# Performance work log

Measured on AMD Instinct MI355X. Metric: run time of the kernel, lower is better.

The kernel has to match this reference:

```python
import jax, jax.numpy as jnp
import numpy as np

NUM_HEADS = 16
ROPE_THETA = 10000.0


def _rope_angles(seq_len, head_dim, dtype):
    # lucidrains rotary_embedding_torch: freqs = theta^(-2i/d) for i in 0..d/2,
    # angles = pos * freq, then each angle repeated twice along last dim (interleaved pairs).
    inv_freq = 1.0 / (ROPE_THETA ** (jnp.arange(0, head_dim, 2, dtype=jnp.float32) / head_dim))
    angles = jnp.arange(seq_len, dtype=jnp.float32)[:, None] * inv_freq  # [N, D/2]
    return jnp.repeat(angles, 2, axis=-1).astype(dtype)  # [N, D]


def _rotate_half(t):
    # interleaved pairs: (x0, x1) -> (-x1, x0)
    t1 = t[..., ::2]
    t2 = t[..., 1::2]
    return jnp.stack([-t2, t1], axis=-1).reshape(t.shape)


def _apply_rope(t, cos, sin):
    # t: [B, H, N, D]; cos/sin: [N, D]
    return t * cos + _rotate_half(t) * sin


def setup_inputs() -> dict:
    key = jax.random.key(0)
    ks = jax.random.split(key, 5)
    B, N, C = 4, 1024, 1024
    return {
        "x": jax.random.normal(ks[0], (B, N, C), dtype=jnp.float32),
        "w_qkv": jax.random.normal(ks[1], (C, 3 * C), dtype=jnp.float32) * (C ** -0.5),
        "b_qkv": jax.random.normal(ks[2], (3 * C,), dtype=jnp.float32) * 0.02,
        "w_proj": jax.random.normal(ks[3], (C, C), dtype=jnp.float32) * (C ** -0.5),
        "b_proj": jax.random.normal(ks[4], (C,), dtype=jnp.float32) * 0.02,
    }


def reference(x, w_qkv, b_qkv, w_proj, b_proj):
    B, N, C = x.shape
    H = NUM_HEADS
    D = C // H

    qkv = x @ w_qkv + b_qkv  # [B, N, 3C]
    qkv = qkv.reshape(B, N, 3, H, D).transpose(2, 0, 3, 1, 4)  # [3, B, H, N, D]
    q, k, v = qkv[0], qkv[1], qkv[2]

    ang = _rope_angles(N, D, x.dtype)
    cos, sin = jnp.cos(ang), jnp.sin(ang)
    q = _apply_rope(q, cos, sin)
    k = _apply_rope(k, cos, sin)

    scale = D ** -0.5  # SDPA default scale
    scores = jnp.einsum("bhqd,bhkd->bhqk", q, k) * scale
    attn = jax.nn.softmax(scores, axis=-1)
    out = jnp.einsum("bhqk,bhkd->bhqd", attn, v)  # [B, H, N, D]

    out = out.transpose(0, 2, 1, 3).reshape(B, N, C)
    return out @ w_proj + b_proj
```

## Files before the change

### kernel.cpp

```cpp
#include <hip/hip_runtime.h>
#include <math.h>

#define BB 4
#define NN 1024
#define CC 1024
#define HH 16
#define DD 64
#define N3 3072

typedef __attribute__((ext_vector_type(8))) short bf16x8;
typedef __attribute__((ext_vector_type(8))) _Float16 f16x8;
typedef __attribute__((ext_vector_type(4))) _Float16 f16x4;
typedef __attribute__((ext_vector_type(4))) float f32x4;

struct ushort4_t { unsigned short x, y, z, w; };

static __device__ __forceinline__ unsigned short f2b(float f) {
    union { float f; unsigned int u; } v; v.f = f;
    unsigned int r = (v.u + 0x7fffu + ((v.u >> 16) & 1u)) >> 16;
    return (unsigned short)r;
}

static __device__ __forceinline__ void ldg_lds16(const void* g, void* l) {
    __builtin_amdgcn_global_load_lds(
        (const __attribute__((address_space(1))) unsigned int*)g,
        (__attribute__((address_space(3))) unsigned int*)l, 16, 0, 0);
}

__global__ __launch_bounds__(256) void prep(const float* __restrict__ x,
                                            const float* __restrict__ wq,
                                            const float* __restrict__ wp,
                                            _Float16* __restrict__ Xh,
                                            _Float16* __restrict__ Wqt,
                                            _Float16* __restrict__ Wpt,
                                            float* __restrict__ ct,
                                            float* __restrict__ st) {
    const int blk = blockIdx.x;
    const int t = threadIdx.x;
    if (blk < 4096) {
        int tid = blk * 256 + t;
        float4 v = ((const float4*)x)[tid];
        f16x4 o = {(_Float16)v.x, (_Float16)v.y, (_Float16)v.z, (_Float16)v.w};
        ((f16x4*)Xh)[tid] = o;
    } else if (blk < 5632) {
        int idx = blk - 4096;
        int n  = (idx % 12) * 256 + t;
        int k0 = (idx / 12) * 8;
        f16x8 o;
        #pragma unroll
        for (int kk = 0; kk < 8; kk++)
            o[kk] = (_Float16)wq[(size_t)(k0 + kk) * N3 + n];
        *(f16x8*)(Wqt + (size_t)n * 1024 + k0) = o;
    } else if (blk < 6144) {
        int idx = blk - 5632;
        int n  = (idx % 4) * 256 + t;
        int k0 = (idx / 4) * 8;
        f16x8 o;
        #pragma unroll
        for (int kk = 0; kk < 8; kk++)
            o[kk] = (_Float16)wp[(size_t)(k0 + kk) * 1024 + n];
        *(f16x8*)(Wpt + (size_t)n * 1024 + k0) = o;
    } else {
        int tid = (blk - 6144) * 256 + t;
        int n = tid >> 5, i = tid & 31;
        double ang = (double)n * exp2(-(double)i * (13.287712379549449 / 32.0));
        ct[tid] = (float)cos(ang);
        st[tid] = (float)sin(ang);
    }
}

static __device__ __forceinline__ void gemm_body_128(const char* gA, const char* gB,
                                                     int m0, int n0,
                                                     _Float16* As, _Float16* Bs,
                                                     int w, int lane, int ln, int qd,
                                                     int wm, int wn, f32x4 acc[4][4]) {
    const int r8 = lane >> 3;
    const int xorc = ((lane & 7) ^ r8) * 16;
    for (int k0 = 0; k0 < 1024; k0 += 64) {
        #pragma unroll
        for (int c = 0; c < 4; c++) {
            int rr = w * 32 + c * 8 + r8;
            ldg_lds16(gA + (size_t)(m0 + rr) * 2048 + k0 * 2 + xorc,
                      &As[(w * 32 + c * 8) * 64]);
            ldg_lds16(gB + (size_t)(n0 + rr) * 2048 + k0 * 2 + xorc,
                      &Bs[(w * 32 + c * 8) * 64]);
        }
        __syncthreads();
        #pragma unroll
        for (int kc = 0; kc < 2; kc++) {
            f16x8 af[4], bf[4];
            #pragma unroll
            for (int i = 0; i < 4; i++)
                af[i] = *(const f16x8*)&As[(wm + i * 16 + ln) * 64 +
                                           (((kc * 4 + qd) ^ (ln & 7)) * 8)];
            #pragma unroll
            for (int j = 0; j < 4; j++)
                bf[j] = *(const f16x8*)&Bs[(wn + j * 16 + ln) * 64 +
                                           (((kc * 4 + qd) ^ (ln & 7)) * 8)];
            #pragma unroll
            for (int i = 0; i < 4; i++)
                #pragma unroll
                for (int j = 0; j < 4; j++)
                    acc[i][j] = __builtin_amdgcn_mfma_f32_16x16x32_f16(af[i], bf[j],
                                                                       acc[i][j], 0, 0, 0);
        }
        __syncthreads();
    }
}

__global__ __launch_bounds__(256) void qkv_mfma(const _Float16* __restrict__ Ah,
                                                const _Float16* __restrict__ Bt,
                                                const float* __restrict__ bias,
                                                const float* __restrict__ cost,
                                                const float* __restrict__ sint,
                                                unsigned short* __restrict__ Q,
                                                unsigned short* __restrict__ K,
                                                unsigned short* __restrict__ Vtg) {
    __shared__ __align__(16) _Float16 As[128 * 64];
    __shared__ __align__(16) _Float16 Bs[128 * 64];
    const int t = threadIdx.x;
    const int lane = t & 63;
    const int w = t >> 6;
    const int ln = lane & 15, qd = lane >> 4;
    const int n0 = blockIdx.x * 128;
    const int m0 = blockIdx.y * 128;
    const int wm = (w >> 1) * 64, wn = (w & 1) * 64;

    f32x4 acc[4][4];
    #pragma unroll
    for (int i = 0; i < 4; i++)
        #pragma unroll
        for (int j = 0; j < 4; j++) acc[i][j] = (f32x4){0.f, 0.f, 0.f, 0.f};

    gemm_body_128((const char*)Ah, (const char*)Bt, m0, n0, As, Bs,
                  w, lane, ln, qd, wm, wn, acc);

    const int s = n0 >> 10;
    const int h = ((n0 + wn) >> 6) & 15;
    if (s < 2) {
        unsigned short* dst = (s == 0) ? Q : K;
        const float sc0 = (s == 0) ? 0.125f : 1.0f;
        #pragma unroll
        for (int i = 0; i < 4; i++) {
            #pragma unroll
            for (int reg = 0; reg < 4; reg++) {
                int row = m0 + wm + i * 16 + qd * 4 + reg;
                int b = row >> 10, n = row & 1023;
                size_t obase = (((size_t)(b * HH + h)) * NN + n) * DD;
                #pragma unroll
                for (int j = 0; j < 4; j++) {
                    int d = j * 16 + ln;
                    float v = acc[i][j][reg] + bias[n0 + wn + d];
                    float pv = __shfl_xor(v, 1);
                    float cs = cost[n * 32 + (d >> 1)];
                    float sn = sint[n * 32 + (d >> 1)];
                    float outv = ((d & 1) ? (v * cs + pv * sn) : (v * cs - pv * sn)) * sc0;
                    dst[obase + d] = f2b(outv);
                }
            }
        }
    } else {
        #pragma unroll
        for (int i = 0; i < 4; i++) {
            int row0 = m0 + wm + i * 16 + qd * 4;
            int b = row0 >> 10, n = row0 & 1023;
            size_t tbase = ((size_t)(b * HH + h)) * DD * NN + n;
            #pragma unroll
            for (int j = 0; j < 4; j++) {
                int d = j * 16 + ln;
                float bb = bias[n0 + wn + d];
                ushort4_t pk;
                pk.x = f2b(acc[i][j][0] + bb);
                pk.y = f2b(acc[i][j][1] + bb);
                pk.z = f2b(acc[i][j][2] + bb);
                pk.w = f2b(acc[i][j][3] + bb);
                *(ushort4_t*)&Vtg[tbase + (size_t)d * NN] = pk;
            }
        }
    }
}

__global__ __launch_bounds__(256) void attn_flash(const unsigned short* __restrict__ Qb,
                                                  const unsigned short* __restrict__ Kb,
                                                  const unsigned short* __restrict__ Vtg,
                                                  _Float16* __restrict__ AO) {
    __shared__ __align__(16) unsigned short Ks[3][64 * 64];
    __shared__ __align__(16) unsigned short Vt[2][64 * 64];
    __shared__ __align__(16) unsigned short Ps[4][16 * 64];

    const int t    = threadIdx.x;
    const int lane = t & 63;
    const int w    = t >> 6;
    const int ln   = lane & 15;
    const int qd   = lane >> 4;
    const int bq   = blockIdx.x;
    const int h    = blockIdx.y;
    const int b    = blockIdx.z;
    const size_t base = (size_t)(b * HH + h) * NN * DD;
    const char* Kc = (const char*)(Kb + base);
    const char* Vc = (const char*)(Vtg + base);
    const int xorc = ((lane & 7) ^ (lane >> 3)) * 16;
    const int r8   = lane >> 3;
    const int wrow = w * 16;

    bf16x8 qf0, qf1;
    {
        const unsigned short* qp = Qb + base + (size_t)(bq * 64 + wrow + ln) * DD + qd * 8;
        qf0 = *(const bf16x8*)qp;
        qf1 = *(const bf16x8*)(qp + 32);
    }

    f32x4 o[5];
    #pragma unroll
    for (int x = 0; x < 5; x++) o[x] = (f32x4){0.f, 0.f, 0.f, 0.f};

    bf16x8 onesf;
    #pragma unroll
    for (int x = 0; x < 8; x++) onesf[x] = (short)0x3F80;

    #pragma unroll
    for (int tile = 0; tile < 3; tile++)
        #pragma unroll
        for (int c = 0; c < 2; c++) {
            int rr = wrow + c * 8 + r8;
            ldg_lds16(Kc + (size_t)(tile * 64 + rr) * 128 + xorc,
                      &Ks[tile][(wrow + c * 8) * 64]);
        }
    #pragma unroll
    for (int tile = 0; tile < 2; tile++)
        #pragma unroll
        for (int c = 0; c < 2; c++) {
            int rr = wrow + c * 8 + r8;
            ldg_lds16(Vc + (size_t)rr * 2048 + (size_t)tile * 128 + xorc,
                      &Vt[tile][(wrow + c * 8) * 64]);
        }
    __syncthreads();

    f32x4 scur[4];
    {
        const unsigned short* KsB = Ks[0];
        #pragma unroll
        for (int j = 0; j < 4; j++) {
            f32x4 sj = {0.f, 0.f, 0.f, 0.f};
            bf16x8 k0f = *(const bf16x8*)&KsB[(ln + 16 * j) * 64 + ((qd ^ (ln & 7)) * 8)];
            bf16x8 k1f = *(const bf16x8*)&KsB[(ln + 16 * j) * 64 + (((4 + qd) ^ (ln & 7)) * 8)];
            sj = __builtin_amdgcn_mfma_f32_16x16x32_bf16(qf0, k0f, sj, 0, 0, 0);
            sj = __builtin_amdgcn_mfma_f32_16x16x32_bf16(qf1, k1f, sj, 0, 0, 0);
            scur[j] = sj;
        }
    }

    const float C1 = 1.44269504f;
    const float C0 = -16.0f * 1.44269504f;

    #pragma unroll
    for (int tt = 0; tt < 16; tt++) {
        f32x4 snext[4];
        if (tt < 15) {
            const unsigned short* KsB = Ks[(tt + 1) % 3];
            #pragma unroll
            for (int j = 0; j < 4; j++) {
                f32x4 sj = {0.f, 0.f, 0.f, 0.f};
                bf16x8 k0f = *(const bf16x8*)&KsB[(ln + 16 * j) * 64 + ((qd ^ (ln & 7)) * 8)];
                bf16x8 k1f = *(const bf16x8*)&KsB[(ln + 16 * j) * 64 + (((4 + qd) ^ (ln & 7)) * 8)];
                sj = __builtin_amdgcn_mfma_f32_16x16x32_bf16(qf0, k0f, sj, 0, 0, 0);
                sj = __builtin_amdgcn_mfma_f32_16x16x32_bf16(qf1, k1f, sj, 0, 0, 0);
                snext[j] = sj;
            }
        }

        unsigned short* PsB = &Ps[w][0];
        #pragma unroll
        for (int j = 0; j < 4; j++) {
            #pragma unroll
            for (int r = 0; r < 4; r++) {
                float p = exp2f(fmaf(scur[j][r], C1, C0));
                union { float f; unsigned int u; } cv; cv.f = p;
                int m = qd * 4 + r;
                PsB[m * 64 + ((((ln >> 3) + 2 * j) ^ (m & 7)) * 8) + (ln & 7)] =
                    (unsigned short)((cv.u + 0x8000u) >> 16);
            }
        }

        {
            const unsigned short* VtB = Vt[tt & 1];
            bf16x8 pf0 = *(const bf16x8*)&PsB[ln * 64 + ((qd ^ (ln & 7)) * 8)];
            bf16x8 pf1 = *(const bf16x8*)&PsB[ln * 64 + (((4 + qd) ^ (ln & 7)) * 8)];
            #pragma unroll
            for (int j = 0; j < 4; j++) {
                bf16x8 v0f = *(const bf16x8*)&VtB[(ln + 16 * j) * 64 + ((qd ^ (ln & 7)) * 8)];
                bf16x8 v1f = *(const bf16x8*)&VtB[(ln + 16 * j) * 64 + (((4 + qd) ^ (ln & 7)) * 8)];
                o[j] = __builtin_amdgcn_mfma_f32_16x16x32_bf16(pf0, v0f, o[j], 0, 0, 0);
                o[j] = __builtin_amdgcn_mfma_f32_16x16x32_bf16(pf1, v1f, o[j], 0, 0, 0);
            }
            o[4] = __builtin_amdgcn_mfma_f32_16x16x32_bf16(pf0, onesf, o[4], 0, 0, 0);
            o[4] = __builtin_amdgcn_mfma_f32_16x16x32_bf16(pf1, onesf, o[4], 0, 0, 0);
        }

        __syncthreads();

        if (tt <= 12) {
            int tile = tt + 3;
            #pragma unroll
            for (int c = 0; c < 2; c++) {
                int rr = wrow + c * 8 + r8;
                ldg_lds16(Kc + (size_t)(tile * 64 + rr) * 128 + xorc,
                          &Ks[tt % 3][(wrow + c * 8) * 64]);
            }
        }
        if (tt <= 13) {
            int tile = tt + 2;
            #pragma unroll
            for (int c = 0; c < 2; c++) {
                int rr = wrow + c * 8 + r8;
                ldg_lds16(Vc + (size_t)rr * 2048 + (size_t)tile * 128 + xorc,
                          &Vt[tt & 1][(wrow + c * 8) * 64]);
            }
        }

        #pragma unroll
        for (int j = 0; j < 4; j++) scur[j] = snext[j];
    }

    #pragma unroll
    for (int r = 0; r < 4; r++) {
        float inv = 1.0f / o[4][r];
        int q = bq * 64 + wrow + qd * 4 + r;
        _Float16* op = AO + (((size_t)b * NN + q) * HH + h) * DD + ln;
        op[0]  = (_Float16)(o[0][r] * inv);
        op[16] = (_Float16)(o[1][r] * inv);
        op[32] = (_Float16)(o[2][r] * inv);
        op[48] = (_Float16)(o[3][r] * inv);
    }
}

__global__ __launch_bounds__(256) void proj_mfma(const _Float16* __restrict__ Ah,
                                                 const _Float16* __restrict__ Bt,
                                                 const float* __restrict__ bias,
                                                 float* __restrict__ out) {
    __shared__ __align__(16) _Float16 As[128 * 64];
    __shared__ __align__(16) _Float16 Bs[128 * 64];
    const int t = threadIdx.x;
    const int lane = t & 63;
    const int w = t >> 6;
    const int ln = lane & 15, qd = lane >> 4;
    const int n0 = blockIdx.x * 128;
    const int m0 = blockIdx.y * 128;
    const int wm = (w >> 1) * 64, wn = (w & 1) * 64;

    f32x4 acc[4][4];
    #pragma unroll
    for (int i = 0; i < 4; i++)
        #pragma unroll
        for (int j = 0; j < 4; j++) acc[i][j] = (f32x4){0.f, 0.f, 0.f, 0.f};

    gemm_body_128((const char*)Ah, (const char*)Bt, m0, n0, As, Bs,
                  w, lane, ln, qd, wm, wn, acc);

    #pragma unroll
    for (int i = 0; i < 4; i++) {
        #pragma unroll
        for (int reg = 0; reg < 4; reg++) {
            int row = m0 + wm + i * 16 + qd * 4 + reg;
            #pragma unroll
            for (int j = 0; j < 4; j++) {
                int col = n0 + wn + j * 16 + ln;
                out[(size_t)row * 1024 + col] = acc[i][j][reg] + bias[col];
            }
        }
    }
}

extern "C" void kernel_launch(void* const* d_in, const int* in_sizes, int n_in,
                              void* d_out, int out_size, void* d_ws, size_t ws_size,
                              hipStream_t stream) {
    const float* x      = (const float*)d_in[0];
    const float* w_qkv  = (const float*)d_in[1];
    const float* b_qkv  = (const float*)d_in[2];
    const float* w_proj = (const float*)d_in[3];
    const float* b_proj = (const float*)d_in[4];
    float* out = (float*)d_out;

    char* ws = (char*)d_ws;
    _Float16* Xh   = (_Float16*)(ws);
    _Float16* Wqt  = (_Float16*)(ws + (8u << 20));
    _Float16* Wpt  = (_Float16*)(ws + (14u << 20));
    unsigned short* Q  = (unsigned short*)(ws + (16u << 20));
    unsigned short* K  = (unsigned short*)(ws + (24u << 20));
    unsigned short* Vt = (unsigned short*)(ws + (32u << 20));
    _Float16* AOh  = (_Float16*)(ws + (40u << 20));
    float* cost    = (float*)(ws + (48u << 20));
    float* sint    = (float*)(ws + (48u << 20) + (128u << 10));

    prep<<<6272, 256, 0, stream>>>(x, w_qkv, w_proj, Xh, Wqt, Wpt, cost, sint);
    qkv_mfma<<<dim3(24, 32), 256, 0, stream>>>(Xh, Wqt, b_qkv, cost, sint, Q, K, Vt);
    attn_flash<<<dim3(16, 16, 4), 256, 0, stream>>>(Q, K, Vt, AOh);
    proj_mfma<<<dim3(8, 32), 256, 0, stream>>>(AOh, Wpt, b_proj, out);
}
```

Before: 199.2 us.

## Double-buffer GEMM LDS tiles with register-staged global prefetch

Replaces the direct global-to-LDS loads in the shared GEMM body with register-staged loads. Two LDS buffers are used so the next K tile is written while the current one is consumed, and the tile after that is prefetched into registers. This cuts the sync count to one barrier per K step and overlaps global latency with MFMA work in both the QKV and projection GEMMs. In exchange, LDS use doubles to 64KB per block and register pressure rises, which may lower occupancy.

```diff
diff --git a/kernel.cpp b/kernel.cpp
--- a/kernel.cpp
+++ b/kernel.cpp
@@ -12,6 +12,7 @@
 typedef __attribute__((ext_vector_type(8))) _Float16 f16x8;
 typedef __attribute__((ext_vector_type(4))) _Float16 f16x4;
 typedef __attribute__((ext_vector_type(4))) float f32x4;
+typedef __attribute__((ext_vector_type(4))) unsigned int u32x4;
 
 struct ushort4_t { unsigned short x, y, z, w; };
 
@@ -69,33 +70,54 @@
     }
 }
 
-static __device__ __forceinline__ void gemm_body_128(const char* gA, const char* gB,
-                                                     int m0, int n0,
-                                                     _Float16* As, _Float16* Bs,
-                                                     int w, int lane, int ln, int qd,
-                                                     int wm, int wn, f32x4 acc[4][4]) {
-    const int r8 = lane >> 3;
-    const int xorc = ((lane & 7) ^ r8) * 16;
-    for (int k0 = 0; k0 < 1024; k0 += 64) {
-        #pragma unroll
-        for (int c = 0; c < 4; c++) {
-            int rr = w * 32 + c * 8 + r8;
-            ldg_lds16(gA + (size_t)(m0 + rr) * 2048 + k0 * 2 + xorc,
-                      &As[(w * 32 + c * 8) * 64]);
-            ldg_lds16(gB + (size_t)(n0 + rr) * 2048 + k0 * 2 + xorc,
-                      &Bs[(w * 32 + c * 8) * 64]);
-        }
-        __syncthreads();
+static __device__ __forceinline__ void gemm_body_pipe(const char* gA, const char* gB,
+                                                      int m0, int n0,
+                                                      _Float16* As0, _Float16* As1,
+                                                      _Float16* Bs0, _Float16* Bs1,
+                                                      int tid, int ln, int qd,
+                                                      int wm, int wn, f32x4 acc[4][4]) {
+    const int lrow   = tid >> 3;
+    const int lchunk = tid & 7;
+    const int swz    = (lchunk ^ (lrow & 7)) * 8;
+
+    u32x4 pa[4], pb[4];
+
+    #pragma unroll
+    for (int c = 0; c < 4; c++) {
+        size_t ra = (size_t)(m0 + c * 32 + lrow) * 2048 + lchunk * 16;
+        size_t rb = (size_t)(n0 + c * 32 + lrow) * 2048 + lchunk * 16;
+        pa[c] = *(const u32x4*)(gA + ra);
+        pb[c] = *(const u32x4*)(gB + rb);
+    }
+    #pragma unroll
+    for (int c = 0; c < 4; c++) {
+        *(u32x4*)&As0[(c * 32 + lrow) * 64 + swz] = pa[c];
+        *(u32x4*)&Bs0[(c * 32 + lrow) * 64 + swz] = pb[c];
+    }
+    #pragma unroll
+    for (int c = 0; c < 4; c++) {
+        size_t ra = (size_t)(m0 + c * 32 + lrow) * 2048 + 128 + lchunk * 16;
+        size_t rb = (size_t)(n0 + c * 32 + lrow) * 2048 + 128 + lchunk * 16;
+        pa[c] = *(const u32x4*)(gA + ra);
+        pb[c] = *(const u32x4*)(gB + rb);
+    }
+    __syncthreads();
+
+    #pragma unroll
+    for (int t = 0; t < 16; t++) {
+        const _Float16* Ac = (t & 1) ? As1 : As0;
+        const _Float16* Bc = (t & 1) ? Bs1 : Bs0;
+
         #pragma unroll
         for (int kc = 0; kc < 2; kc++) {
             f16x8 af[4], bf[4];
             #pragma unroll
             for (int i = 0; i < 4; i++)
-                af[i] = *(const f16x8*)&As[(wm + i * 16 + ln) * 64 +
+                af[i] = *(const f16x8*)&Ac[(wm + i * 16 + ln) * 64 +
                                            (((kc * 4 + qd) ^ (ln & 7)) * 8)];
             #pragma unroll
             for (int j = 0; j < 4; j++)
-                bf[j] = *(const f16x8*)&Bs[(wn + j * 16 + ln) * 64 +
+                bf[j] = *(const f16x8*)&Bc[(wn + j * 16 + ln) * 64 +
                                            (((kc * 4 + qd) ^ (ln & 7)) * 8)];
             #pragma unroll
             for (int i = 0; i < 4; i++)
@@ -103,6 +125,26 @@
                 for (int j = 0; j < 4; j++)
                     acc[i][j] = __builtin_amdgcn_mfma_f32_16x16x32_f16(af[i], bf[j],
                                                                        acc[i][j], 0, 0, 0);
+        }
+
+        if (t < 15) {
+            _Float16* An = (t & 1) ? As0 : As1;
+            _Float16* Bn = (t & 1) ? Bs0 : Bs1;
+            #pragma unroll
+            for (int c = 0; c < 4; c++) {
+                *(u32x4*)&An[(c * 32 + lrow) * 64 + swz] = pa[c];
+                *(u32x4*)&Bn[(c * 32 + lrow) * 64 + swz] = pb[c];
+            }
+            if (t < 14) {
+                size_t ko = (size_t)(t + 2) * 128;
+                #pragma unroll
+                for (int c = 0; c < 4; c++) {
+                    size_t ra = (size_t)(m0 + c * 32 + lrow) * 2048 + ko + lchunk * 16;
+                    size_t rb = (size_t)(n0 + c * 32 + lrow) * 2048 + ko + lchunk * 16;
+                    pa[c] = *(const u32x4*)(gA + ra);
+                    pb[c] = *(const u32x4*)(gB + rb);
+                }
+            }
         }
         __syncthreads();
     }
@@ -116,8 +158,8 @@
                                                 unsigned short* __restrict__ Q,
                                                 unsigned short* __restrict__ K,
                                                 unsigned short* __restrict__ Vtg) {
-    __shared__ __align__(16) _Float16 As[128 * 64];
-    __shared__ __align__(16) _Float16 Bs[128 * 64];
+    __shared__ __align__(16) _Float16 As[2][128 * 64];
+    __shared__ __align__(16) _Float16 Bs[2][128 * 64];
     const int t = threadIdx.x;
     const int lane = t & 63;
     const int w = t >> 6;
@@ -132,8 +174,8 @@
         #pragma unroll
         for (int j = 0; j < 4; j++) acc[i][j] = (f32x4){0.f, 0.f, 0.f, 0.f};
 
-    gemm_body_128((const char*)Ah, (const char*)Bt, m0, n0, As, Bs,
-                  w, lane, ln, qd, wm, wn, acc);
+    gemm_body_pipe((const char*)Ah, (const char*)Bt, m0, n0,
+                   As[0], As[1], Bs[0], Bs[1], t, ln, qd, wm, wn, acc);
 
     const int s = n0 >> 10;
     const int h = ((n0 + wn) >> 6) & 15;
@@ -338,8 +380,8 @@
                                                  const _Float16* __restrict__ Bt,
                                                  const float* __restrict__ bias,
                                                  float* __restrict__ out) {
-    __shared__ __align__(16) _Float16 As[128 * 64];
-    __shared__ __align__(16) _Float16 Bs[128 * 64];
+    __shared__ __align__(16) _Float16 As[2][128 * 64];
+    __shared__ __align__(16) _Float16 Bs[2][128 * 64];
     const int t = threadIdx.x;
     const int lane = t & 63;
     const int w = t >> 6;
@@ -354,8 +396,8 @@
         #pragma unroll
         for (int j = 0; j < 4; j++) acc[i][j] = (f32x4){0.f, 0.f, 0.f, 0.f};
 
-    gemm_body_128((const char*)Ah, (const char*)Bt, m0, n0, As, Bs,
-                  w, lane, ln, qd, wm, wn, acc);
+    gemm_body_pipe((const char*)Ah, (const char*)Bt, m0, n0,
+                   As[0], As[1], Bs[0], Bs[1], t, ln, qd, wm, wn, acc);
 
     #pragma unroll
     for (int i = 0; i < 4; i++) {
```

Measured after the change: 185.7 us. 1.07x faster.
